# Kernel tuning notes

Measured on AMD Instinct MI355X. Metric: run time of the kernel, lower is better.

The kernel has to match this reference:

```python
import jax, jax.numpy as jnp
from jax import lax
import numpy as np

SAMPLE_RATIO = 0.25
K = 20          # nsample from group_args
SLOPE = 0.2     # leakyrelu negative_slope
EPS = 1e-5      # BatchNorm eps


def fps(p, m):
    """Furthest point sampling. p: [B,N,3] -> idx [B,m] int32."""
    B, N, _ = p.shape

    def step(carry, _):
        dist, last_idx = carry                      # [B,N], [B]
        last_pt = jnp.take_along_axis(p, last_idx[:, None, None], axis=1)  # [B,1,3]
        d = jnp.sum((p - last_pt) ** 2, axis=-1)    # [B,N]
        dist = jnp.minimum(dist, d)
        nxt = jnp.argmax(dist, axis=1).astype(jnp.int32)
        return (dist, nxt), last_idx

    dist0 = jnp.full((B, N), 1e10, dtype=p.dtype)
    idx0 = jnp.zeros((B,), dtype=jnp.int32)
    _, idxs = lax.scan(step, (dist0, idx0), None, length=m)
    return jnp.transpose(idxs)                      # [B,m]


def knn_idx(q, p, k):
    """q: [B,M,3] queries, p: [B,N,3] -> [B,M,k] indices of k nearest."""
    # squared distances, [B,M,N] (the memory-bound intermediate)
    d = (jnp.sum(q * q, -1)[:, :, None]
         + jnp.sum(p * p, -1)[:, None, :]
         - 2.0 * jnp.einsum('bmd,bnd->bmn', q, p))
    _, idx = lax.top_k(-d, k)
    return idx


def convblock(x, W, g, b):
    """1x1 Conv2d (bias=False) -> leakyrelu(0.2) -> BatchNorm2d (train-mode)."""
    x = jnp.einsum('oc,bcmk->bomk', W, x)
    x = jnp.where(x >= 0, x, SLOPE * x)
    mean = jnp.mean(x, axis=(0, 2, 3), keepdims=True)
    var = jnp.var(x, axis=(0, 2, 3), keepdims=True)
    return g[None, :, None, None] * (x - mean) * lax.rsqrt(var + EPS) + b[None, :, None, None]


def setup_inputs() -> dict:
    key = jax.random.key(0)
    ks = jax.random.split(key, 4)
    C = 64
    p = jax.random.normal(ks[0], (4, 8192, 3), dtype=jnp.float32)
    # kaiming-normal-ish conv weights (1x1 kernels flattened to [out,in])
    W1 = jax.random.normal(ks[1], (C, 6), dtype=jnp.float32) * np.sqrt(2.0 / 6)
    W2 = jax.random.normal(ks[2], (C, C), dtype=jnp.float32) * np.sqrt(2.0 / C)
    W3 = jax.random.normal(ks[3], (C, C), dtype=jnp.float32) * np.sqrt(2.0 / C)
    ones = jnp.ones((C,), jnp.float32)
    zeros = jnp.zeros((C,), jnp.float32)
    return {"p": p, "W1": W1, "g1": ones, "b1": zeros,
            "W2": W2, "g2": ones, "b2": zeros,
            "W3": W3, "g3": ones, "b3": zeros}


def reference(p, W1, g1, b1, W2, g2, b2, W3, g3, b3):
    B, N, _ = p.shape
    M = int(N * SAMPLE_RATIO)
    # features default to xyz: f = p^T, [B,3,N]; we keep [B,N,3] layout for gathers
    idx = fps(p, M)                                              # [B,M]
    p1 = jnp.take_along_axis(p, idx[:, :, None], axis=1)         # [B,M,3]
    nidx = knn_idx(p1, p, K)                                     # [B,M,K]
    batch = jnp.arange(B)[:, None, None]
    grouped = p[batch, nidx]                                     # [B,M,K,3] gathered xyz (== gathered features)
    dp = grouped - p1[:, :, None, :]                             # [B,M,K,3] relative coords
    # cat((dp, gf), dim=1) in channel-first layout -> [B,6,M,K]
    gf = jnp.concatenate([dp, grouped], axis=-1)                 # [B,M,K,6]
    x = jnp.transpose(gf, (0, 3, 1, 2))                          # [B,6,M,K]
    x = convblock(x, W1, g1, b1)
    x = convblock(x, W2, g2, b2)
    x = convblock(x, W3, g3, b3)
    return jnp.max(x, axis=-1)                                   # [B,64,M]
```

## Files before the change

### kernel.cpp

```cpp
#include <hip/hip_runtime.h>
#include <cstdint>
#include <cstddef>


#define B_ 4
#define N_ 8192
#define M_ 2048
#define K_ 20
#define BMK (B_*M_*K_)
#define EPS_ 1e-5f
#define TILE_ 1024
#define PERS 248

typedef unsigned long long ull;
typedef float f32x2 __attribute__((ext_vector_type(2)));

__device__ __forceinline__ ull packkey(float d, int idx) {
  unsigned int bb = __float_as_uint(d);
  bb ^= (bb & 0x80000000u) ? 0xFFFFFFFFu : 0x80000000u;
  return ((ull)bb << 32) | (unsigned int)idx;
}
__device__ __forceinline__ float keymaxf(ull k) {
  unsigned int hb = (unsigned int)(k >> 32);
  unsigned int fb = (hb & 0x80000000u) ? (hb ^ 0x80000000u) : ~hb;
  return __uint_as_float(fb);
}
__device__ __forceinline__ void insert20(ull* keys, ull key) {
#pragma unroll
  for (int i = 19; i > 0; --i) {
    ull lo = keys[i-1];
    keys[i] = (key < lo) ? lo : ((key < keys[i]) ? key : keys[i]);
  }
  keys[0] = (key < keys[0]) ? key : keys[0];
}

#define DPPMAXU(V, CTRL) {                                                           \
    unsigned int nh = (unsigned int)__builtin_amdgcn_update_dpp(                     \
        (int)V, (int)V, CTRL, 0xF, 0xF, false);                                      \
    V = (nh > V) ? nh : V; }

__global__ __launch_bounds__(512)
void fpsknn_kernel(const float* __restrict__ p, float* __restrict__ p1,
                   float* __restrict__ gfp, const float* __restrict__ W1,
                   float* __restrict__ stats, int* __restrict__ prog) {
  __shared__ union {
    struct { float4 pts4[N_]; unsigned int slotsv[2][8]; int idxsel[2]; } f;
    struct { float4 tile[TILE_]; ull mk[8*32*20]; float bs[128]; } k;
  } sm;
  const int tid = threadIdx.x;

  if (blockIdx.x < B_) {
#pragma clang fp contract(off)
    const int b = blockIdx.x;
    const float* pb = p + (size_t)b * (N_*3);
    float* p1b = p1 + (size_t)b * (M_*3);
    float4* pts4 = sm.f.pts4;
    const int wv = tid >> 6;
    const int base = tid * 16;
    f32x2 X[8], Y[8], Z[8], D[8];
#pragma unroll
    for (int j = 0; j < 8; ++j) {
      int i = base + 2*j;
      float x0 = pb[i*3+0], y0 = pb[i*3+1], z0 = pb[i*3+2];
      float x1 = pb[i*3+3], y1 = pb[i*3+4], z1 = pb[i*3+5];
      X[j] = (f32x2){x0, x1};
      Y[j] = (f32x2){y0, y1};
      Z[j] = (f32x2){z0, z1};
      D[j] = (f32x2){1e10f, 1e10f};
      pts4[i]   = make_float4(x0, y0, z0, 0.f);
      pts4[i+1] = make_float4(x1, y1, z1, 0.f);
    }
    if (tid < 2) sm.f.idxsel[tid] = 0x7FFFFFFF;
    float qx = pb[0], qy = pb[1], qz = pb[2];
    if (tid == 0) { p1b[0] = qx; p1b[1] = qy; p1b[2] = qz; }
    __syncthreads();
    for (int t = 1; t < M_; ++t) {
      const int cur = t & 1;
      f32x2 q2x = (f32x2){qx, qx};
      f32x2 q2y = (f32x2){qy, qy};
      f32x2 q2z = (f32x2){qz, qz};
      f32x2 tmx = (f32x2){-1.f, -1.f};
#pragma unroll
      for (int j = 0; j < 8; ++j) {
        f32x2 dx = X[j] - q2x;
        f32x2 dy = Y[j] - q2y;
        f32x2 dz = Z[j] - q2z;
        f32x2 s = (dx*dx + dy*dy) + dz*dz;
        f32x2 dj = __builtin_elementwise_min(D[j], s);
        D[j] = dj;
        tmx = __builtin_elementwise_max(tmx, dj);
      }
      float tm = fmaxf(tmx.x, tmx.y);
      const unsigned int tmb = __float_as_uint(tm);
      unsigned int hv = tmb;
      DPPMAXU(hv, 0x111)
      DPPMAXU(hv, 0x112)
      DPPMAXU(hv, 0x114)
      DPPMAXU(hv, 0x118)
      DPPMAXU(hv, 0x142)
      DPPMAXU(hv, 0x143)
      if ((tid & 63) == 63) sm.f.slotsv[cur][wv] = hv;
      __syncthreads();
      if (tid == 0) sm.f.idxsel[cur ^ 1] = 0x7FFFFFFF;
      unsigned int g = sm.f.slotsv[cur][0];
#pragma unroll
      for (int j = 1; j < 8; ++j) { unsigned int s2 = sm.f.slotsv[cur][j]; g = (s2 > g) ? s2 : g; }
      if (tmb == g) {
        int fj = 0x7FFFFFFF;
#pragma unroll
        for (int j = 7; j >= 0; --j) {
          if (__float_as_uint(D[j].y) == g) fj = base + 2*j + 1;
          if (__float_as_uint(D[j].x) == g) fj = base + 2*j;
        }
        atomicMin(&sm.f.idxsel[cur], fj);
      }
      __syncthreads();
      int sel = sm.f.idxsel[cur];
      sel = __builtin_amdgcn_readfirstlane(sel);
      float4 qv = pts4[sel];
      qx = qv.x; qy = qv.y; qz = qv.z;
      if (tid == 0) {
        p1b[t*3+0] = qx; p1b[t*3+1] = qy; p1b[t*3+2] = qz;
        if ((t & 63) == 63)
          __hip_atomic_store(&prog[b], t, __ATOMIC_RELEASE, __HIP_MEMORY_SCOPE_AGENT);
      }
    }
    if (tid == 0)
      __hip_atomic_store(&prog[b], M_, __ATOMIC_RELEASE, __HIP_MEMORY_SCOPE_AGENT);
    return;
  }

  float4* tile = sm.k.tile;
  ull* mk = sm.k.mk;
  float* gfl = (float*)sm.k.tile;
  float* bs = sm.k.bs;
  for (int ord = (int)blockIdx.x - B_; ord < 1024; ord += PERS) {
    const int b = ord & 3;
    const int q0 = (ord >> 2) * 8;
    if (tid == 0) {
      while (__hip_atomic_load(&prog[b], __ATOMIC_ACQUIRE, __HIP_MEMORY_SCOPE_AGENT) < q0 + 7)
        __builtin_amdgcn_s_sleep(16);
    }
    __syncthreads();
    { int pv = __hip_atomic_load(&prog[b], __ATOMIC_ACQUIRE, __HIP_MEMORY_SCOPE_AGENT);
      asm volatile("" :: "v"(pv)); }

    const int ql = (tid >> 5) & 7;
    const int part = tid & 31;
    const int m = q0 + ql;
    const float* pb = p + (size_t)b*(N_*3);
    const float* qp_ = p1 + ((size_t)b*M_ + m)*3;
    float qx = qp_[0], qy = qp_[1], qz = qp_[2];
    float qq = __fadd_rn(__fadd_rn(__fmul_rn(qx,qx), __fmul_rn(qy,qy)), __fmul_rn(qz,qz));
    ull keys[20];
#pragma unroll
    for (int i = 0; i < 20; ++i) keys[i] = 0xFF8000007FFFFFFFull;
    float maxf = __uint_as_float(0x7F800000u);
    for (int t0 = 0; t0 < N_; t0 += TILE_) {
      __syncthreads();
      for (int i = tid; i < TILE_; i += 512) {
        float x = pb[(t0+i)*3+0], y = pb[(t0+i)*3+1], z = pb[(t0+i)*3+2];
        float pp = __fadd_rn(__fadd_rn(__fmul_rn(x,x), __fmul_rn(y,y)), __fmul_rn(z,z));
        tile[i] = make_float4(x, y, z, pp);
      }
      __syncthreads();
      if (tid < 256) {
        const int sbase = part * 32;
        for (int s = 0; s < 32; ++s) {
          int ss = sbase + ((s + part) & 31);
          float4 pt = tile[ss];
          float qp = fmaf(pt.z, qz, fmaf(pt.y, qy, __fmul_rn(pt.x, qx)));
          float d = __fsub_rn(__fadd_rn(qq, pt.w), __fmul_rn(2.0f, qp));
          if (d <= maxf) {
            ull key = packkey(d, t0 + ss);
            if (key < keys[19]) { insert20(keys, key); maxf = keymaxf(keys[19]); }
          }
        }
      }
    }
    if (tid < 256) {
      ull* myslot = &mk[(ql*32 + part)*20];
#pragma unroll
      for (int i = 0; i < 20; ++i) myslot[i] = keys[i];
    }
    __syncthreads();
    if (tid < 256 && part == 0) {
      for (int pp2 = 1; pp2 < 32; ++pp2) {
        const ull* os = &mk[(ql*32 + pp2)*20];
        for (int i = 0; i < 20; ++i) {
          ull k = os[i];
          if (k >= keys[19]) break;
          insert20(keys, k);
        }
      }
      ull* myslot = &mk[(ql*32)*20];
#pragma unroll
      for (int i = 0; i < 20; ++i) myslot[i] = keys[i];
    }
    __syncthreads();
    for (int w = tid; w < 8*K_; w += 512) {
      int ql2 = w / K_;
      int kk = w - ql2*K_;
      ull key = mk[ql2*32*20 + kk];
      int idx = (int)(unsigned int)(key & 0xFFFFFFFFu);
      float gx = pb[idx*3+0], gy = pb[idx*3+1], gz = pb[idx*3+2];
      int m2 = q0 + ql2;
      const float* qv = p1 + ((size_t)b*M_ + m2)*3;
      size_t col = ((size_t)(b*M_ + m2))*K_ + kk;
      float d0 = __fsub_rn(gx, qv[0]);
      float d1 = __fsub_rn(gy, qv[1]);
      float d2 = __fsub_rn(gz, qv[2]);
      gfp[0*BMK + col] = d0;
      gfp[1*BMK + col] = d1;
      gfp[2*BMK + col] = d2;
      gfp[3*BMK + col] = gx;
      gfp[4*BMK + col] = gy;
      gfp[5*BMK + col] = gz;
      gfl[w*6+0] = d0; gfl[w*6+1] = d1; gfl[w*6+2] = d2;
      gfl[w*6+3] = gx; gfl[w*6+4] = gy; gfl[w*6+5] = gz;
    }
    __syncthreads();
    {
      const int lane = tid & 63;
      const int grp = tid >> 6;
      float w1r[6];
#pragma unroll
      for (int c = 0; c < 6; ++c) w1r[c] = W1[lane*6 + c];
      float acc = 0.f, accq = 0.f;
      for (int cc = 0; cc < 20; ++cc) {
        const float* gv = &gfl[(grp*20 + cc)*6];
        float y = __fmul_rn(w1r[0], gv[0]);
#pragma unroll
        for (int c = 1; c < 6; ++c) y = fmaf(w1r[c], gv[c], y);
        float u = (y >= 0.f) ? y : 0.2f*y;
        acc += u;
        accq = fmaf(u, u, accq);
      }
      if (tid < 128) bs[tid] = 0.f;
      __syncthreads();
      atomicAdd(&bs[lane], acc);
      atomicAdd(&bs[64+lane], accq);
      __syncthreads();
      if (tid < 128) atomicAdd(&stats[tid], bs[tid]);
    }
  }
}

__device__ __forceinline__ void bn_coeff(const float* __restrict__ st,
                                         const float* __restrict__ g,
                                         const float* __restrict__ bb,
                                         int o, float& A, float& C) {
  const float inv = 1.0f / (float)BMK;
  float mean = st[o] * inv;
  float var  = st[64+o] * inv - mean*mean;
  float a = g[o] / sqrtf(var + EPS_);
  A = a;
  C = fmaf(-a, mean, bb[o]);
}

__global__ __launch_bounds__(256) void convB_kernel(const float* __restrict__ gfp,
                                                    const float* __restrict__ W1,
                                                    const float* __restrict__ stats,
                                                    const float* __restrict__ g1,
                                                    const float* __restrict__ b1,
                                                    const float* __restrict__ W2,
                                                    float* __restrict__ u2t) {
  __shared__ float sA[64], sC[64];
  const int tid = threadIdx.x;
  if (tid < 64) bn_coeff(stats, g1, b1, tid, sA[tid], sC[tid]);
  __syncthreads();
  const int col = blockIdx.x * 256 + tid;
  float gf[6];
#pragma unroll
  for (int c = 0; c < 6; ++c) gf[c] = gfp[c*BMK + col];
  float x1[64];
#pragma unroll
  for (int c = 0; c < 64; ++c) {
    float y = __fmul_rn(W1[c*6+0], gf[0]);
#pragma unroll
    for (int i = 1; i < 6; ++i) y = fmaf(W1[c*6+i], gf[i], y);
    float u = (y >= 0.f) ? y : 0.2f*y;
    x1[c] = fmaf(sA[c], u, sC[c]);
  }
  float* ob = u2t + (size_t)col * 64;
  for (int o4 = 0; o4 < 16; ++o4) {
    float y0 = 0.f, y1 = 0.f, y2 = 0.f, y3 = 0.f;
#pragma unroll
    for (int c = 0; c < 64; ++c) {
      float xc = x1[c];
      y0 = fmaf(W2[(o4*4+0)*64+c], xc, y0);
      y1 = fmaf(W2[(o4*4+1)*64+c], xc, y1);
      y2 = fmaf(W2[(o4*4+2)*64+c], xc, y2);
      y3 = fmaf(W2[(o4*4+3)*64+c], xc, y3);
    }
    float4 v;
    v.x = (y0 >= 0.f) ? y0 : 0.2f*y0;
    v.y = (y1 >= 0.f) ? y1 : 0.2f*y1;
    v.z = (y2 >= 0.f) ? y2 : 0.2f*y2;
    v.w = (y3 >= 0.f) ? y3 : 0.2f*y3;
    ((float4*)ob)[o4] = v;
  }
}

__global__ __launch_bounds__(256) void stats2_kernel(const float* __restrict__ u2t,
                                                     float* __restrict__ stats) {
  const int g = blockIdx.x * 256 + threadIdx.x;
  const int ntot = gridDim.x * 256;
  const float4* u4 = (const float4*)u2t;
  const int nf4 = BMK * 16;
  float a0=0,a1=0,a2=0,a3=0,s0=0,s1=0,s2=0,s3=0;
  for (int i = g; i < nf4; i += ntot) {
    float4 v = u4[i];
    a0 += v.x; s0 = fmaf(v.x, v.x, s0);
    a1 += v.y; s1 = fmaf(v.y, v.y, s1);
    a2 += v.z; s2 = fmaf(v.z, v.z, s2);
    a3 += v.w; s3 = fmaf(v.w, v.w, s3);
  }
  const int c0 = (4*g) & 63;
  __shared__ float bs[128];
  if (threadIdx.x < 128) bs[threadIdx.x] = 0.f;
  __syncthreads();
  atomicAdd(&bs[c0+0], a0); atomicAdd(&bs[c0+1], a1);
  atomicAdd(&bs[c0+2], a2); atomicAdd(&bs[c0+3], a3);
  atomicAdd(&bs[64+c0+0], s0); atomicAdd(&bs[64+c0+1], s1);
  atomicAdd(&bs[64+c0+2], s2); atomicAdd(&bs[64+c0+3], s3);
  __syncthreads();
  if (threadIdx.x < 128) atomicAdd(&stats[threadIdx.x], bs[threadIdx.x]);
}

__global__ __launch_bounds__(256) void stats3_kernel(const float* __restrict__ u2t,
                                                     const float* __restrict__ W3,
                                                     const float* __restrict__ stats2v,
                                                     const float* __restrict__ g2,
                                                     const float* __restrict__ b2,
                                                     float* __restrict__ stats) {
  __shared__ float sA2[64], sC2[64];
  const int tid = threadIdx.x;
  if (tid < 64) bn_coeff(stats2v, g2, b2, tid, sA2[tid], sC2[tid]);
  __syncthreads();
  const int lane = tid & 63;
  float w[64];
#pragma unroll
  for (int c = 0; c < 64; ++c) w[c] = W3[lane*64 + c] * sA2[c];
  float bb = 0.f;
#pragma unroll
  for (int c = 0; c < 64; ++c) bb = fmaf(W3[lane*64 + c], sC2[c], bb);
  const int gw = (blockIdx.x*256 + tid) >> 6;
  const int nw = (gridDim.x*256) >> 6;
  float acc = 0.f, accq = 0.f;
  for (int col = gw; col < BMK; col += nw) {
    const float4* u4 = (const float4*)(u2t + (size_t)col*64);
    float y = bb;
#pragma unroll
    for (int c4 = 0; c4 < 16; ++c4) {
      float4 v = u4[c4];
      y = fmaf(w[4*c4+0], v.x, y);
      y = fmaf(w[4*c4+1], v.y, y);
      y = fmaf(w[4*c4+2], v.z, y);
      y = fmaf(w[4*c4+3], v.w, y);
    }
    float u = (y >= 0.f) ? y : 0.2f*y;
    acc += u; accq = fmaf(u, u, accq);
  }
  __shared__ float bs[128];
  if (tid < 128) bs[tid] = 0.f;
  __syncthreads();
  atomicAdd(&bs[lane], acc);
  atomicAdd(&bs[64+lane], accq);
  __syncthreads();
  if (tid < 128) atomicAdd(&stats[tid], bs[tid]);
}

__global__ __launch_bounds__(256) void out_kernel(const float* __restrict__ u2t,
                                                  const float* __restrict__ W3,
                                                  const float* __restrict__ stats2v,
                                                  const float* __restrict__ g2,
                                                  const float* __restrict__ b2,
                                                  const float* __restrict__ stats3v,
                                                  const float* __restrict__ g3,
                                                  const float* __restrict__ b3,
                                                  float* __restrict__ out) {
  __shared__ float sA2[64], sC2[64];
  const int tid = threadIdx.x;
  if (tid < 64) bn_coeff(stats2v, g2, b2, tid, sA2[tid], sC2[tid]);
  __syncthreads();
  const int lane = tid & 63;
  const int wv = (blockIdx.x*256 + tid) >> 6;
  float w[64];
#pragma unroll
  for (int c = 0; c < 64; ++c) w[c] = W3[lane*64 + c] * sA2[c];
  float bb = 0.f;
#pragma unroll
  for (int c = 0; c < 64; ++c) bb = fmaf(W3[lane*64 + c], sC2[c], bb);
  float mx = -3.4e38f, mn = 3.4e38f;
  for (int k = 0; k < K_; ++k) {
    const float4* u4 = (const float4*)(u2t + ((size_t)wv*K_ + k)*64);
    float y = bb;
#pragma unroll
    for (int c4 = 0; c4 < 16; ++c4) {
      float4 v = u4[c4];
      y = fmaf(w[4*c4+0], v.x, y);
      y = fmaf(w[4*c4+1], v.y, y);
      y = fmaf(w[4*c4+2], v.z, y);
      y = fmaf(w[4*c4+3], v.w, y);
    }
    float u = (y >= 0.f) ? y : 0.2f*y;
    mx = fmaxf(mx, u); mn = fminf(mn, u);
  }
  float A3, C3;
  bn_coeff(stats3v, g3, b3, lane, A3, C3);
  float r = (A3 >= 0.f) ? mx : mn;
  int b = wv >> 11, m = wv & 2047;
  out[((size_t)(b*64 + lane))*M_ + m] = fmaf(A3, r, C3);
}

extern "C" void kernel_launch(void* const* d_in, const int* in_sizes, int n_in,
                              void* d_out, int out_size, void* d_ws, size_t ws_size,
                              hipStream_t stream) {
  const float* p  = (const float*)d_in[0];
  const float* W1 = (const float*)d_in[1];
  const float* g1 = (const float*)d_in[2];
  const float* b1 = (const float*)d_in[3];
  const float* W2 = (const float*)d_in[4];
  const float* g2 = (const float*)d_in[5];
  const float* b2 = (const float*)d_in[6];
  const float* W3 = (const float*)d_in[7];
  const float* g3 = (const float*)d_in[8];
  const float* b3 = (const float*)d_in[9];
  float* out = (float*)d_out;
  char* ws = (char*)d_ws;

  float* p1    = (float*)(ws);
  float* gfp   = (float*)(ws + 131072);
  float* u2t   = (float*)(ws + 4194304);
  float* stats = (float*)(ws + 46137344);
  int*   prog  = (int*)(ws + 46138880);

  hipMemsetAsync((void*)stats, 0, 1552, stream);
  hipLaunchKernelGGL(fpsknn_kernel, dim3(B_ + PERS), dim3(512), 0, stream,
                     p, p1, gfp, W1, stats, prog);
  hipLaunchKernelGGL(convB_kernel,  dim3(640),  dim3(256), 0, stream, gfp, W1, stats, g1, b1, W2, u2t);
  hipLaunchKernelGGL(stats2_kernel, dim3(512),  dim3(256), 0, stream, u2t, stats+128);
  hipLaunchKernelGGL(stats3_kernel, dim3(512),  dim3(256), 0, stream, u2t, W3, stats+128, g2, b2, stats+256);
  hipLaunchKernelGGL(out_kernel,    dim3(2048), dim3(256), 0, stream, u2t, W3, stats+128, g2, b2, stats+256, g3, b3, out);
}
```

Baseline: 2.457 ms.

## Fuse conv/stats/output tail kernels into one persistent kernel with grid barriers

Replaces the four post-FPS/KNN kernels (convB, stats2, stats3, out) with a single persistent 256-block kernel whose phases are separated by atomic-counter grid barriers. The aim is to remove the launch gaps between kernels and to reuse the W3-derived per-lane weights across the last two phases. In exchange, each phase now runs on only 256 blocks with grid-stride loops, which lowers occupancy compared with the earlier 640- and 2048-block launches. Correctness also depends on all 256 blocks being co-resident so the spin barriers cannot deadlock.

```diff
diff --git a/kernel.cpp b/kernel.cpp
--- a/kernel.cpp
+++ b/kernel.cpp
@@ -258,160 +258,152 @@
   C = fmaf(-a, mean, bb[o]);
 }
 
-__global__ __launch_bounds__(256) void convB_kernel(const float* __restrict__ gfp,
-                                                    const float* __restrict__ W1,
-                                                    const float* __restrict__ stats,
-                                                    const float* __restrict__ g1,
-                                                    const float* __restrict__ b1,
-                                                    const float* __restrict__ W2,
-                                                    float* __restrict__ u2t) {
+__device__ __forceinline__ void gridbar(int* c, int expected) {
+  __syncthreads();
+  if (threadIdx.x == 0) {
+    __hip_atomic_fetch_add(c, 1, __ATOMIC_ACQ_REL, __HIP_MEMORY_SCOPE_AGENT);
+    while (__hip_atomic_load(c, __ATOMIC_ACQUIRE, __HIP_MEMORY_SCOPE_AGENT) < expected)
+      __builtin_amdgcn_s_sleep(2);
+  }
+  __syncthreads();
+}
+
+__global__ __launch_bounds__(256)
+void tail_kernel(const float* __restrict__ gfp, const float* __restrict__ W1,
+                 float* __restrict__ stats,
+                 const float* __restrict__ g1, const float* __restrict__ b1,
+                 const float* __restrict__ W2, float* __restrict__ u2t,
+                 const float* __restrict__ W3,
+                 const float* __restrict__ g2, const float* __restrict__ b2,
+                 const float* __restrict__ g3, const float* __restrict__ b3,
+                 float* __restrict__ out, int* __restrict__ bar) {
+  const int tid = threadIdx.x;
+  const int nthr = (int)gridDim.x * 256;
+  const int nblk = (int)gridDim.x;
   __shared__ float sA[64], sC[64];
-  const int tid = threadIdx.x;
+  __shared__ float bs[128];
+
   if (tid < 64) bn_coeff(stats, g1, b1, tid, sA[tid], sC[tid]);
   __syncthreads();
-  const int col = blockIdx.x * 256 + tid;
-  float gf[6];
-#pragma unroll
-  for (int c = 0; c < 6; ++c) gf[c] = gfp[c*BMK + col];
-  float x1[64];
-#pragma unroll
-  for (int c = 0; c < 64; ++c) {
-    float y = __fmul_rn(W1[c*6+0], gf[0]);
-#pragma unroll
-    for (int i = 1; i < 6; ++i) y = fmaf(W1[c*6+i], gf[i], y);
-    float u = (y >= 0.f) ? y : 0.2f*y;
-    x1[c] = fmaf(sA[c], u, sC[c]);
-  }
-  float* ob = u2t + (size_t)col * 64;
-  for (int o4 = 0; o4 < 16; ++o4) {
-    float y0 = 0.f, y1 = 0.f, y2 = 0.f, y3 = 0.f;
+  for (int col = (int)blockIdx.x*256 + tid; col < BMK; col += nthr) {
+    float gf[6];
+#pragma unroll
+    for (int c = 0; c < 6; ++c) gf[c] = gfp[c*BMK + col];
+    float x1[64];
 #pragma unroll
     for (int c = 0; c < 64; ++c) {
-      float xc = x1[c];
-      y0 = fmaf(W2[(o4*4+0)*64+c], xc, y0);
-      y1 = fmaf(W2[(o4*4+1)*64+c], xc, y1);
-      y2 = fmaf(W2[(o4*4+2)*64+c], xc, y2);
-      y3 = fmaf(W2[(o4*4+3)*64+c], xc, y3);
-    }
-    float4 v;
-    v.x = (y0 >= 0.f) ? y0 : 0.2f*y0;
-    v.y = (y1 >= 0.f) ? y1 : 0.2f*y1;
-    v.z = (y2 >= 0.f) ? y2 : 0.2f*y2;
-    v.w = (y3 >= 0.f) ? y3 : 0.2f*y3;
-    ((float4*)ob)[o4] = v;
-  }
-}
-
-__global__ __launch_bounds__(256) void stats2_kernel(const float* __restrict__ u2t,
-                                                     float* __restrict__ stats) {
-  const int g = blockIdx.x * 256 + threadIdx.x;
-  const int ntot = gridDim.x * 256;
-  const float4* u4 = (const float4*)u2t;
-  const int nf4 = BMK * 16;
-  float a0=0,a1=0,a2=0,a3=0,s0=0,s1=0,s2=0,s3=0;
-  for (int i = g; i < nf4; i += ntot) {
-    float4 v = u4[i];
-    a0 += v.x; s0 = fmaf(v.x, v.x, s0);
-    a1 += v.y; s1 = fmaf(v.y, v.y, s1);
-    a2 += v.z; s2 = fmaf(v.z, v.z, s2);
-    a3 += v.w; s3 = fmaf(v.w, v.w, s3);
-  }
-  const int c0 = (4*g) & 63;
-  __shared__ float bs[128];
-  if (threadIdx.x < 128) bs[threadIdx.x] = 0.f;
-  __syncthreads();
-  atomicAdd(&bs[c0+0], a0); atomicAdd(&bs[c0+1], a1);
-  atomicAdd(&bs[c0+2], a2); atomicAdd(&bs[c0+3], a3);
-  atomicAdd(&bs[64+c0+0], s0); atomicAdd(&bs[64+c0+1], s1);
-  atomicAdd(&bs[64+c0+2], s2); atomicAdd(&bs[64+c0+3], s3);
-  __syncthreads();
-  if (threadIdx.x < 128) atomicAdd(&stats[threadIdx.x], bs[threadIdx.x]);
-}
-
-__global__ __launch_bounds__(256) void stats3_kernel(const float* __restrict__ u2t,
-                                                     const float* __restrict__ W3,
-                                                     const float* __restrict__ stats2v,
-                                                     const float* __restrict__ g2,
-                                                     const float* __restrict__ b2,
-                                                     float* __restrict__ stats) {
-  __shared__ float sA2[64], sC2[64];
-  const int tid = threadIdx.x;
-  if (tid < 64) bn_coeff(stats2v, g2, b2, tid, sA2[tid], sC2[tid]);
-  __syncthreads();
+      float y = __fmul_rn(W1[c*6+0], gf[0]);
+#pragma unroll
+      for (int i = 1; i < 6; ++i) y = fmaf(W1[c*6+i], gf[i], y);
+      float u = (y >= 0.f) ? y : 0.2f*y;
+      x1[c] = fmaf(sA[c], u, sC[c]);
+    }
+    float* ob = u2t + (size_t)col * 64;
+    for (int o4 = 0; o4 < 16; ++o4) {
+      float y0 = 0.f, y1 = 0.f, y2 = 0.f, y3 = 0.f;
+#pragma unroll
+      for (int c = 0; c < 64; ++c) {
+        float xc = x1[c];
+        y0 = fmaf(W2[(o4*4+0)*64+c], xc, y0);
+        y1 = fmaf(W2[(o4*4+1)*64+c], xc, y1);
+        y2 = fmaf(W2[(o4*4+2)*64+c], xc, y2);
+        y3 = fmaf(W2[(o4*4+3)*64+c], xc, y3);
+      }
+      float4 v;
+      v.x = (y0 >= 0.f) ? y0 : 0.2f*y0;
+      v.y = (y1 >= 0.f) ? y1 : 0.2f*y1;
+      v.z = (y2 >= 0.f) ? y2 : 0.2f*y2;
+      v.w = (y3 >= 0.f) ? y3 : 0.2f*y3;
+      ((float4*)ob)[o4] = v;
+    }
+  }
+  gridbar(&bar[0], nblk);
+
+  {
+    const float4* u4 = (const float4*)u2t;
+    const int nf4 = BMK * 16;
+    float a0=0,a1=0,a2=0,a3=0,s0=0,s1=0,s2=0,s3=0;
+    for (int i = (int)blockIdx.x*256 + tid; i < nf4; i += nthr) {
+      float4 v = u4[i];
+      a0 += v.x; s0 = fmaf(v.x, v.x, s0);
+      a1 += v.y; s1 = fmaf(v.y, v.y, s1);
+      a2 += v.z; s2 = fmaf(v.z, v.z, s2);
+      a3 += v.w; s3 = fmaf(v.w, v.w, s3);
+    }
+    const int c0 = (4*tid) & 63;
+    if (tid < 128) bs[tid] = 0.f;
+    __syncthreads();
+    atomicAdd(&bs[c0+0], a0); atomicAdd(&bs[c0+1], a1);
+    atomicAdd(&bs[c0+2], a2); atomicAdd(&bs[c0+3], a3);
+    atomicAdd(&bs[64+c0+0], s0); atomicAdd(&bs[64+c0+1], s1);
+    atomicAdd(&bs[64+c0+2], s2); atomicAdd(&bs[64+c0+3], s3);
+    __syncthreads();
+    if (tid < 128) atomicAdd(&stats[128 + tid], bs[tid]);
+  }
+  gridbar(&bar[1], nblk);
+
   const int lane = tid & 63;
   float w[64];
-#pragma unroll
-  for (int c = 0; c < 64; ++c) w[c] = W3[lane*64 + c] * sA2[c];
   float bb = 0.f;
-#pragma unroll
-  for (int c = 0; c < 64; ++c) bb = fmaf(W3[lane*64 + c], sC2[c], bb);
-  const int gw = (blockIdx.x*256 + tid) >> 6;
-  const int nw = (gridDim.x*256) >> 6;
-  float acc = 0.f, accq = 0.f;
-  for (int col = gw; col < BMK; col += nw) {
-    const float4* u4 = (const float4*)(u2t + (size_t)col*64);
-    float y = bb;
-#pragma unroll
-    for (int c4 = 0; c4 < 16; ++c4) {
-      float4 v = u4[c4];
-      y = fmaf(w[4*c4+0], v.x, y);
-      y = fmaf(w[4*c4+1], v.y, y);
-      y = fmaf(w[4*c4+2], v.z, y);
-      y = fmaf(w[4*c4+3], v.w, y);
-    }
-    float u = (y >= 0.f) ? y : 0.2f*y;
-    acc += u; accq = fmaf(u, u, accq);
-  }
-  __shared__ float bs[128];
-  if (tid < 128) bs[tid] = 0.f;
-  __syncthreads();
-  atomicAdd(&bs[lane], acc);
-  atomicAdd(&bs[64+lane], accq);
-  __syncthreads();
-  if (tid < 128) atomicAdd(&stats[tid], bs[tid]);
-}
-
-__global__ __launch_bounds__(256) void out_kernel(const float* __restrict__ u2t,
-                                                  const float* __restrict__ W3,
-                                                  const float* __restrict__ stats2v,
-                                                  const float* __restrict__ g2,
-                                                  const float* __restrict__ b2,
-                                                  const float* __restrict__ stats3v,
-                                                  const float* __restrict__ g3,
-                                                  const float* __restrict__ b3,
-                                                  float* __restrict__ out) {
-  __shared__ float sA2[64], sC2[64];
-  const int tid = threadIdx.x;
-  if (tid < 64) bn_coeff(stats2v, g2, b2, tid, sA2[tid], sC2[tid]);
-  __syncthreads();
-  const int lane = tid & 63;
-  const int wv = (blockIdx.x*256 + tid) >> 6;
-  float w[64];
-#pragma unroll
-  for (int c = 0; c < 64; ++c) w[c] = W3[lane*64 + c] * sA2[c];
-  float bb = 0.f;
-#pragma unroll
-  for (int c = 0; c < 64; ++c) bb = fmaf(W3[lane*64 + c], sC2[c], bb);
-  float mx = -3.4e38f, mn = 3.4e38f;
-  for (int k = 0; k < K_; ++k) {
-    const float4* u4 = (const float4*)(u2t + ((size_t)wv*K_ + k)*64);
-    float y = bb;
-#pragma unroll
-    for (int c4 = 0; c4 < 16; ++c4) {
-      float4 v = u4[c4];
-      y = fmaf(w[4*c4+0], v.x, y);
-      y = fmaf(w[4*c4+1], v.y, y);
-      y = fmaf(w[4*c4+2], v.z, y);
-      y = fmaf(w[4*c4+3], v.w, y);
-    }
-    float u = (y >= 0.f) ? y : 0.2f*y;
-    mx = fmaxf(mx, u); mn = fminf(mn, u);
-  }
-  float A3, C3;
-  bn_coeff(stats3v, g3, b3, lane, A3, C3);
-  float r = (A3 >= 0.f) ? mx : mn;
-  int b = wv >> 11, m = wv & 2047;
-  out[((size_t)(b*64 + lane))*M_ + m] = fmaf(A3, r, C3);
+  {
+    if (tid < 64) bn_coeff(stats + 128, g2, b2, tid, sA[tid], sC[tid]);
+    __syncthreads();
+#pragma unroll
+    for (int c = 0; c < 64; ++c) w[c] = W3[lane*64 + c] * sA[c];
+#pragma unroll
+    for (int c = 0; c < 64; ++c) bb = fmaf(W3[lane*64 + c], sC[c], bb);
+    const int gw = ((int)blockIdx.x*256 + tid) >> 6;
+    const int nw = nthr >> 6;
+    float acc = 0.f, accq = 0.f;
+    for (int col = gw; col < BMK; col += nw) {
+      const float4* u4 = (const float4*)(u2t + (size_t)col*64);
+      float y = bb;
+#pragma unroll
+      for (int c4 = 0; c4 < 16; ++c4) {
+        float4 v = u4[c4];
+        y = fmaf(w[4*c4+0], v.x, y);
+        y = fmaf(w[4*c4+1], v.y, y);
+        y = fmaf(w[4*c4+2], v.z, y);
+        y = fmaf(w[4*c4+3], v.w, y);
+      }
+      float u = (y >= 0.f) ? y : 0.2f*y;
+      acc += u; accq = fmaf(u, u, accq);
+    }
+    if (tid < 128) bs[tid] = 0.f;
+    __syncthreads();
+    atomicAdd(&bs[lane], acc);
+    atomicAdd(&bs[64+lane], accq);
+    __syncthreads();
+    if (tid < 128) atomicAdd(&stats[256 + tid], bs[tid]);
+  }
+  gridbar(&bar[2], nblk);
+
+  {
+    float A3, C3;
+    bn_coeff(stats + 256, g3, b3, lane, A3, C3);
+    const int w0 = ((int)blockIdx.x*256 + tid) >> 6;
+    const int nw = nthr >> 6;
+    for (int wv = w0; wv < B_*M_; wv += nw) {
+      float mx = -3.4e38f, mn = 3.4e38f;
+      for (int k = 0; k < K_; ++k) {
+        const float4* u4 = (const float4*)(u2t + ((size_t)wv*K_ + k)*64);
+        float y = bb;
+#pragma unroll
+        for (int c4 = 0; c4 < 16; ++c4) {
+          float4 v = u4[c4];
+          y = fmaf(w[4*c4+0], v.x, y);
+          y = fmaf(w[4*c4+1], v.y, y);
+          y = fmaf(w[4*c4+2], v.z, y);
+          y = fmaf(w[4*c4+3], v.w, y);
+        }
+        float u = (y >= 0.f) ? y : 0.2f*y;
+        mx = fmaxf(mx, u); mn = fminf(mn, u);
+      }
+      float r = (A3 >= 0.f) ? mx : mn;
+      int b = wv >> 11, m = wv & 2047;
+      out[((size_t)(b*64 + lane))*M_ + m] = fmaf(A3, r, C3);
+    }
+  }
 }
 
 extern "C" void kernel_launch(void* const* d_in, const int* in_sizes, int n_in,
@@ -435,12 +427,11 @@
   float* u2t   = (float*)(ws + 4194304);
   float* stats = (float*)(ws + 46137344);
   int*   prog  = (int*)(ws + 46138880);
-
-  hipMemsetAsync((void*)stats, 0, 1552, stream);
+  int*   bar   = (int*)(ws + 46138896);
+
+  hipMemsetAsync((void*)stats, 0, 1568, stream);
   hipLaunchKernelGGL(fpsknn_kernel, dim3(B_ + PERS), dim3(512), 0, stream,
                      p, p1, gfp, W1, stats, prog);
-  hipLaunchKernelGGL(convB_kernel,  dim3(640),  dim3(256), 0, stream, gfp, W1, stats, g1, b1, W2, u2t);
-  hipLaunchKernelGGL(stats2_kernel, dim3(512),  dim3(256), 0, stream, u2t, stats+128);
-  hipLaunchKernelGGL(stats3_kernel, dim3(512),  dim3(256), 0, stream, u2t, W3, stats+128, g2, b2, stats+256);
-  hipLaunchKernelGGL(out_kernel,    dim3(2048), dim3(256), 0, stream, u2t, W3, stats+128, g2, b2, stats+256, g3, b3, out);
-}
+  hipLaunchKernelGGL(tail_kernel,   dim3(256), dim3(256), 0, stream,
+                     gfp, W1, stats, g1, b1, W2, u2t, W3, g2, b2, g3, b3, out, bar);
+}
```

Result: slower. 2.514 ms (+2.3%).
